# Performance work log

Hardware: AMD Instinct MI355X
Metric: run time of the kernel (lower is better)

Reference implementation:

```python
import jax, jax.numpy as jnp
import numpy as np

ALPHA = 0.8
GAMMA = 2.0
SMOOTH = 1e-4
FOCAL_W = 20.0
DICE_W = 1.0
IOU_W = 1.0
MASK_THRESH = 0.0
AREA_RANGES = np.array([[0.0, 0.04], [0.01, 0.16], [0.09, 0.49], [0.25, 1.0]], dtype=np.float32)
B, K, H, W = 128, 4, 256, 256


def setup_inputs() -> dict:
    key = jax.random.key(0)
    k1, k2, k3, k4 = jax.random.split(key, 4)
    pred_masks = jax.random.normal(k1, (B, K, H, W), dtype=jnp.float32)
    pred_ious = jax.random.uniform(k2, (B, K), dtype=jnp.float32)
    # binary targets with varying per-sample foreground density so different
    # samples fall into different area_ranges (exercises the branching)
    dens = jax.random.uniform(k3, (B, 1, 1, 1), dtype=jnp.float32)
    noise = jax.random.uniform(k4, (B, 1, H, W), dtype=jnp.float32)
    targets = (noise < dens).astype(jnp.float32)
    return {"pred_masks": pred_masks, "pred_ious": pred_ious, "targets": targets}


def _aggregate(loss_bk, valid_bk):
    # per-sample mean over valid idxs, then mean over samples with >=1 valid idx
    cnt = valid_bk.sum(axis=1)                                   # [B]
    per_sample = (loss_bk * valid_bk).sum(axis=1) / jnp.maximum(cnt, 1.0)
    per_sample = jnp.where(cnt > 0, per_sample, 0.0)
    vb = (cnt > 0).astype(loss_bk.dtype).sum()
    total = per_sample.sum()
    return jnp.where(vb > 0, total / jnp.maximum(vb, 1.0), total)


def _compute(pred_masks, pred_ious, targets):
    b = pred_masks.shape[0]
    x = pred_masks.reshape(b, K, -1)                             # [B,K,HW] logits
    t = targets.reshape(b, -1)                                   # [B,HW] binary
    hw = t.shape[1]
    ratio = t.sum(axis=1) / float(hw)                            # [B]
    lo = jnp.asarray(AREA_RANGES[:, 0])
    hi = jnp.asarray(AREA_RANGES[:, 1])
    valid = ((ratio[:, None] > lo[None, :]) & (ratio[:, None] < hi[None, :])).astype(x.dtype)  # [B,K]

    tb = t[:, None, :]                                           # [B,1,HW]
    # focal: stable BCE-with-logits, elementwise
    bce = jnp.maximum(x, 0.0) - x * tb + jnp.log1p(jnp.exp(-jnp.abs(x)))
    focal_bk = (ALPHA * (1.0 - jnp.exp(-bce)) ** GAMMA * bce).mean(axis=2)  # [B,K]
    focal = FOCAL_W * _aggregate(focal_bk, valid)

    # dice on clamped sigmoid probabilities
    p = jnp.clip(jax.nn.sigmoid(x), 1e-4, 1.0 - 1e-4)
    inter = (p * tb).sum(axis=2)                                 # [B,K]
    dice_bk = 1.0 - (2.0 * inter + SMOOTH) / (p.sum(axis=2) + t.sum(axis=1)[:, None] + SMOOTH)
    dice = DICE_W * _aggregate(dice_bk, valid)

    # iou prediction loss on thresholded masks
    m = (x >= MASK_THRESH).astype(x.dtype)
    i2 = (m * tb).sum(axis=2)
    iou_gt = (i2 + SMOOTH) / (m.sum(axis=2) + t.sum(axis=1)[:, None] - i2 + SMOOTH)
    iou_bk = (pred_ious - iou_gt) ** 2                           # [B,K]
    iou = IOU_W * _aggregate(iou_bk, valid)

    return focal, dice, iou


def reference(pred_masks, pred_ious, targets):
    focal, dice, iou = _compute(pred_masks, pred_ious, targets)
    return focal, dice, iou
```

## Files before the change

kernel.cpp:

```cpp
#include <hip/hip_runtime.h>
#include <math.h>

#define B_   128
#define K_   4
#define HW_  65536

constexpr int BLOCK  = 256;
constexpr int CHUNK  = 4096;
constexpr int NCHUNK = HW_ / CHUNK;
constexpr int V4_PER_THREAD = CHUNK / 4 / BLOCK;

__device__ __forceinline__ void proc_elem(float x, float t,
                                          float& fs, float& in, float& ps,
                                          float& i2, float& ms) {
    float e   = __expf(-fabsf(x));
    float inv = __builtin_amdgcn_rcpf(1.0f + e);
    bool  pos = (x >= 0.0f);
    float s   = pos ? inv : 1.0f - inv;
    float nms = fmaf(-2.0f, s, 1.0f);
    float pt  = fmaf(t, nms, s);
    float l   = __logf(pt);
    float om  = 1.0f - pt;
    fs = fmaf(om * om * l, -0.8f, fs);
    float pc  = fminf(fmaxf(s, 1e-4f), 0.9999f);
    ps += pc;
    in  = fmaf(pc, t, in);
    float m = pos ? 1.0f : 0.0f;
    ms += m;
    i2  = fmaf(m, t, i2);
}

__global__ __launch_bounds__(BLOCK) void partial_kernel(
    const float* __restrict__ pred_masks,
    const float* __restrict__ targets,
    float* __restrict__ fsum,
    float* __restrict__ inter,
    float* __restrict__ psum,
    float* __restrict__ i2s,
    float* __restrict__ msum,
    float* __restrict__ tsum)
{
    const int blk  = blockIdx.x;
    const int b    = blk / NCHUNK;
    const int c    = blk % NCHUNK;
    const int base = c * CHUNK;

    const float4* __restrict__ t4 =
        reinterpret_cast<const float4*>(targets + (size_t)b * HW_ + base);
    const float* __restrict__ xbase = pred_masks + (size_t)b * K_ * HW_ + base;

    float fs[K_] = {0.f, 0.f, 0.f, 0.f};
    float in[K_] = {0.f, 0.f, 0.f, 0.f};
    float ps[K_] = {0.f, 0.f, 0.f, 0.f};
    float i2[K_] = {0.f, 0.f, 0.f, 0.f};
    float ms[K_] = {0.f, 0.f, 0.f, 0.f};
    float ts = 0.f;

    #pragma unroll
    for (int i = 0; i < V4_PER_THREAD; ++i) {
        const int idx = threadIdx.x + i * BLOCK;
        const float4 tv = t4[idx];
        ts += tv.x + tv.y + tv.z + tv.w;
        #pragma unroll
        for (int k = 0; k < K_; ++k) {
            const float4 xv =
                reinterpret_cast<const float4*>(xbase + (size_t)k * HW_)[idx];
            proc_elem(xv.x, tv.x, fs[k], in[k], ps[k], i2[k], ms[k]);
            proc_elem(xv.y, tv.y, fs[k], in[k], ps[k], i2[k], ms[k]);
            proc_elem(xv.z, tv.z, fs[k], in[k], ps[k], i2[k], ms[k]);
            proc_elem(xv.w, tv.w, fs[k], in[k], ps[k], i2[k], ms[k]);
        }
    }

    float vals[21];
    #pragma unroll
    for (int k = 0; k < K_; ++k) {
        vals[k]      = fs[k];
        vals[4 + k]  = in[k];
        vals[8 + k]  = ps[k];
        vals[12 + k] = i2[k];
        vals[16 + k] = ms[k];
    }
    vals[20] = ts;

    const int lane = threadIdx.x & 63;
    const int wave = threadIdx.x >> 6;

    #pragma unroll
    for (int v = 0; v < 21; ++v) {
        float x = vals[v];
        #pragma unroll
        for (int off = 32; off > 0; off >>= 1) x += __shfl_down(x, off, 64);
        vals[v] = x;
    }

    __shared__ float smem[21 * 4];
    if (lane == 0) {
        #pragma unroll
        for (int v = 0; v < 21; ++v) smem[v * 4 + wave] = vals[v];
    }
    __syncthreads();

    if (threadIdx.x < 21) {
        const int v = threadIdx.x;
        const float x = smem[v * 4 + 0] + smem[v * 4 + 1] +
                        smem[v * 4 + 2] + smem[v * 4 + 3];
        float* dst;
        if      (v < 4)  dst = &fsum[b * K_ + v];
        else if (v < 8)  dst = &inter[b * K_ + (v - 4)];
        else if (v < 12) dst = &psum[b * K_ + (v - 8)];
        else if (v < 16) dst = &i2s[b * K_ + (v - 12)];
        else if (v < 20) dst = &msum[b * K_ + (v - 16)];
        else             dst = &tsum[b];
        atomicAdd(dst, x);
    }
}

__global__ __launch_bounds__(128) void finalize_kernel(
    const float* __restrict__ pred_ious,
    const float* __restrict__ fsum,
    const float* __restrict__ inter,
    const float* __restrict__ psum,
    const float* __restrict__ i2s,
    const float* __restrict__ msum,
    const float* __restrict__ tsum,
    float* __restrict__ out)
{
    const float lo[K_] = {0.00f, 0.01f, 0.09f, 0.25f};
    const float hi[K_] = {0.04f, 0.16f, 0.49f, 1.00f};
    const float SMOOTH = 0.0001f;

    const int b = threadIdx.x;
    const float ts = tsum[b];
    const float ratio = ts * (1.0f / (float)HW_);

    float cnt = 0.f, fA = 0.f, dA = 0.f, iA = 0.f;
    #pragma unroll
    for (int k = 0; k < K_; ++k) {
        const bool valid = (ratio > lo[k]) && (ratio < hi[k]);
        if (valid) {
            cnt += 1.0f;
            fA += fsum[b * K_ + k] * (1.0f / (float)HW_);
            const float in_ = inter[b * K_ + k];
            const float ps_ = psum[b * K_ + k];
            dA += 1.0f - (2.0f * in_ + SMOOTH) / (ps_ + ts + SMOOTH);
            const float i2_ = i2s[b * K_ + k];
            const float ms_ = msum[b * K_ + k];
            const float gt  = (i2_ + SMOOTH) / (ms_ + ts - i2_ + SMOOTH);
            const float d   = pred_ious[b * K_ + k] - gt;
            iA += d * d;
        }
    }
    const float invc = (cnt > 0.f) ? (1.0f / cnt) : 0.0f;
    fA *= invc; dA *= invc; iA *= invc;
    float vb = (cnt > 0.f) ? 1.0f : 0.0f;

    float vals[4] = {fA, dA, iA, vb};
    const int lane = threadIdx.x & 63;
    const int wave = threadIdx.x >> 6;
    #pragma unroll
    for (int v = 0; v < 4; ++v) {
        float x = vals[v];
        #pragma unroll
        for (int off = 32; off > 0; off >>= 1) x += __shfl_down(x, off, 64);
        vals[v] = x;
    }
    __shared__ float smem[4 * 2];
    if (lane == 0) {
        #pragma unroll
        for (int v = 0; v < 4; ++v) smem[v * 2 + wave] = vals[v];
    }
    __syncthreads();
    if (threadIdx.x == 0) {
        const float fT  = smem[0] + smem[1];
        const float dT  = smem[2] + smem[3];
        const float iT  = smem[4] + smem[5];
        const float vbT = smem[6] + smem[7];
        const float scale = (vbT > 0.f) ? (1.0f / vbT) : 1.0f;
        out[0] = 20.0f * fT * scale;
        out[1] = dT * scale;
        out[2] = iT * scale;
    }
}

extern "C" void kernel_launch(void* const* d_in, const int* in_sizes, int n_in,
                              void* d_out, int out_size, void* d_ws, size_t ws_size,
                              hipStream_t stream) {
    const float* pred_masks = (const float*)d_in[0];
    const float* pred_ious  = (const float*)d_in[1];
    const float* targets    = (const float*)d_in[2];
    float* out = (float*)d_out;

    float* ws    = (float*)d_ws;
    float* fsum  = ws;
    float* inter = ws + 512;
    float* psum  = ws + 1024;
    float* i2s   = ws + 1536;
    float* msum  = ws + 2048;
    float* tsum  = ws + 2560;

    hipMemsetAsync(d_ws, 0, 2688 * sizeof(float), stream);

    partial_kernel<<<B_ * NCHUNK, BLOCK, 0, stream>>>(
        pred_masks, targets, fsum, inter, psum, i2s, msum, tsum);
    finalize_kernel<<<1, 128, 0, stream>>>(
        pred_ious, fsum, inter, psum, i2s, msum, tsum, out);
}
```

Before: 226.5 us.

## Split partial reduction per mask channel and reduce accumulators per block

```diff
diff --git a/kernel.cpp b/kernel.cpp
--- a/kernel.cpp
+++ b/kernel.cpp
@@ -5,10 +5,10 @@
 #define K_   4
 #define HW_  65536
 
-constexpr int BLOCK  = 256;
-constexpr int CHUNK  = 4096;
-constexpr int NCHUNK = HW_ / CHUNK;
-constexpr int V4_PER_THREAD = CHUNK / 4 / BLOCK;
+constexpr int BLOCK = 256;
+constexpr int NC    = 8;
+constexpr int CHUNK = HW_ / NC;
+constexpr int V4    = CHUNK / 4 / BLOCK;
 
 __device__ __forceinline__ void proc_elem(float x, float t,
                                           float& fs, float& in, float& ps,
@@ -30,7 +30,7 @@
     i2  = fmaf(m, t, i2);
 }
 
-__global__ __launch_bounds__(BLOCK) void partial_kernel(
+__global__ __launch_bounds__(BLOCK, 8) void partial_kernel(
     const float* __restrict__ pred_masks,
     const float* __restrict__ targets,
     float* __restrict__ fsum,
@@ -40,77 +40,62 @@
     float* __restrict__ msum,
     float* __restrict__ tsum)
 {
-    const int blk  = blockIdx.x;
-    const int b    = blk / NCHUNK;
-    const int c    = blk % NCHUNK;
-    const int base = c * CHUNK;
+    const int blk = blockIdx.x;
+    const int k   = blk & (K_ - 1);
+    const int bc  = blk >> 2;
+    const int c   = bc & (NC - 1);
+    const int b   = bc >> 3;
 
     const float4* __restrict__ t4 =
-        reinterpret_cast<const float4*>(targets + (size_t)b * HW_ + base);
-    const float* __restrict__ xbase = pred_masks + (size_t)b * K_ * HW_ + base;
+        reinterpret_cast<const float4*>(targets + (size_t)b * HW_ + c * CHUNK);
+    const float4* __restrict__ x4 =
+        reinterpret_cast<const float4*>(pred_masks +
+            ((size_t)(b * K_ + k)) * HW_ + c * CHUNK);
 
-    float fs[K_] = {0.f, 0.f, 0.f, 0.f};
-    float in[K_] = {0.f, 0.f, 0.f, 0.f};
-    float ps[K_] = {0.f, 0.f, 0.f, 0.f};
-    float i2[K_] = {0.f, 0.f, 0.f, 0.f};
-    float ms[K_] = {0.f, 0.f, 0.f, 0.f};
-    float ts = 0.f;
+    float fs = 0.f, in = 0.f, ps = 0.f, i2 = 0.f, ms = 0.f, ts = 0.f;
 
     #pragma unroll
-    for (int i = 0; i < V4_PER_THREAD; ++i) {
+    for (int i = 0; i < V4; ++i) {
         const int idx = threadIdx.x + i * BLOCK;
         const float4 tv = t4[idx];
+        const float4 xv = x4[idx];
+        proc_elem(xv.x, tv.x, fs, in, ps, i2, ms);
+        proc_elem(xv.y, tv.y, fs, in, ps, i2, ms);
+        proc_elem(xv.z, tv.z, fs, in, ps, i2, ms);
+        proc_elem(xv.w, tv.w, fs, in, ps, i2, ms);
         ts += tv.x + tv.y + tv.z + tv.w;
-        #pragma unroll
-        for (int k = 0; k < K_; ++k) {
-            const float4 xv =
-                reinterpret_cast<const float4*>(xbase + (size_t)k * HW_)[idx];
-            proc_elem(xv.x, tv.x, fs[k], in[k], ps[k], i2[k], ms[k]);
-            proc_elem(xv.y, tv.y, fs[k], in[k], ps[k], i2[k], ms[k]);
-            proc_elem(xv.z, tv.z, fs[k], in[k], ps[k], i2[k], ms[k]);
-            proc_elem(xv.w, tv.w, fs[k], in[k], ps[k], i2[k], ms[k]);
-        }
     }
 
-    float vals[21];
-    #pragma unroll
-    for (int k = 0; k < K_; ++k) {
-        vals[k]      = fs[k];
-        vals[4 + k]  = in[k];
-        vals[8 + k]  = ps[k];
-        vals[12 + k] = i2[k];
-        vals[16 + k] = ms[k];
-    }
-    vals[20] = ts;
-
+    float vals[6] = {fs, in, ps, i2, ms, ts};
     const int lane = threadIdx.x & 63;
     const int wave = threadIdx.x >> 6;
 
     #pragma unroll
-    for (int v = 0; v < 21; ++v) {
+    for (int v = 0; v < 6; ++v) {
         float x = vals[v];
         #pragma unroll
         for (int off = 32; off > 0; off >>= 1) x += __shfl_down(x, off, 64);
         vals[v] = x;
     }
 
-    __shared__ float smem[21 * 4];
+    __shared__ float smem[6 * 4];
     if (lane == 0) {
         #pragma unroll
-        for (int v = 0; v < 21; ++v) smem[v * 4 + wave] = vals[v];
+        for (int v = 0; v < 6; ++v) smem[v * 4 + wave] = vals[v];
     }
     __syncthreads();
 
-    if (threadIdx.x < 21) {
+    if (threadIdx.x < 6) {
         const int v = threadIdx.x;
         const float x = smem[v * 4 + 0] + smem[v * 4 + 1] +
                         smem[v * 4 + 2] + smem[v * 4 + 3];
+        const int bk = b * K_ + k;
         float* dst;
-        if      (v < 4)  dst = &fsum[b * K_ + v];
-        else if (v < 8)  dst = &inter[b * K_ + (v - 4)];
-        else if (v < 12) dst = &psum[b * K_ + (v - 8)];
-        else if (v < 16) dst = &i2s[b * K_ + (v - 12)];
-        else if (v < 20) dst = &msum[b * K_ + (v - 16)];
+        if      (v == 0) dst = &fsum[bk];
+        else if (v == 1) dst = &inter[bk];
+        else if (v == 2) dst = &psum[bk];
+        else if (v == 3) dst = &i2s[bk];
+        else if (v == 4) dst = &msum[bk];
         else             dst = &tsum[b];
         atomicAdd(dst, x);
     }
@@ -131,7 +116,7 @@
     const float SMOOTH = 0.0001f;
 
     const int b = threadIdx.x;
-    const float ts = tsum[b];
+    const float ts = tsum[b] * 0.25f;
     const float ratio = ts * (1.0f / (float)HW_);
 
     float cnt = 0.f, fA = 0.f, dA = 0.f, iA = 0.f;
@@ -201,7 +186,7 @@
 
     hipMemsetAsync(d_ws, 0, 2688 * sizeof(float), stream);
 
-    partial_kernel<<<B_ * NCHUNK, BLOCK, 0, stream>>>(
+    partial_kernel<<<B_ * NC * K_, BLOCK, 0, stream>>>(
         pred_masks, targets, fsum, inter, psum, i2s, msum, tsum);
     finalize_kernel<<<1, 128, 0, stream>>>(
         pred_ious, fsum, inter, psum, i2s, msum, tsum, out);
```

Result: faster. 221.3 us (-2.3%).
